# Kernel tuning notes

Measured on AMD Instinct MI355X. Metric: run time of the kernel, lower is better.

The kernel has to match this reference:

```python
import jax, jax.numpy as jnp
import numpy as np
from jax import lax

D = 256      # key/query dim
D_F = 256    # diff feature channels
C_TOK = 1    # leading context tokens in query_vit
EPS = 1e-6


def conv2d(x, w, b, pad):
    out = lax.conv_general_dilated(x, w, (1, 1), [(pad, pad), (pad, pad)],
                                   dimension_numbers=('NCHW', 'OIHW', 'NCHW'))
    return out + b[None, :, None, None]


def gn1(x, g, b):
    # GroupNorm with 1 group: normalize over (C,H,W) per sample
    mu = jnp.mean(x, axis=(1, 2, 3), keepdims=True)
    var = jnp.var(x, axis=(1, 2, 3), keepdims=True)
    xn = (x - mu) * lax.rsqrt(var + EPS)
    return xn * g[None, :, None, None] + b[None, :, None, None]


def resize_bilinear_ac(x, Ho, Wo):
    # F.interpolate(mode='bilinear', align_corners=True)
    B, C, H, W = x.shape
    ys = jnp.linspace(0.0, H - 1.0, Ho)
    xs = jnp.linspace(0.0, W - 1.0, Wo)
    y0 = jnp.floor(ys).astype(jnp.int32)
    y1 = jnp.minimum(y0 + 1, H - 1)
    wy = (ys - y0)[None, None, :, None]
    x0 = jnp.floor(xs).astype(jnp.int32)
    x1 = jnp.minimum(x0 + 1, W - 1)
    wx = (xs - x0)[None, None, None, :]
    r = x[:, :, y0, :] * (1.0 - wy) + x[:, :, y1, :] * wy
    return r[:, :, :, x0] * (1.0 - wx) + r[:, :, :, x1] * wx


def setup_inputs() -> dict:
    key = jax.random.key(0)
    ks = jax.random.split(key, 12)
    B, Hd, Wd, Ht, Wt = 8, 64, 64, 32, 32

    def kaiming(k, shape, fan_in):
        return jax.random.normal(k, shape, jnp.float32) * np.sqrt(2.0 / fan_in)

    return {
        'query_vit': jax.random.normal(ks[0], (B, C_TOK + Ht * Wt, D), jnp.float32),
        'feat_diff_cat': jax.random.normal(ks[1], (B, 5 * D_F, Hd, Wd), jnp.float32),
        'rb_w1': kaiming(ks[2], (D_F, 5 * D_F, 3, 3), 5 * D_F * 9), 'rb_b1': jnp.zeros((D_F,), jnp.float32),
        'rb_w2': kaiming(ks[3], (D_F, D_F, 3, 3), D_F * 9), 'rb_b2': jnp.zeros((D_F,), jnp.float32),
        'rb_ws': kaiming(ks[4], (D_F, 5 * D_F, 1, 1), 5 * D_F), 'rb_bs': jnp.zeros((D_F,), jnp.float32),
        'ln_g': jnp.ones((D_F,), jnp.float32), 'ln_b': jnp.zeros((D_F,), jnp.float32),
        'key_w': kaiming(ks[5], (D, D_F, 1, 1), D_F), 'key_b': jnp.zeros((D,), jnp.float32),
        'val_w': kaiming(ks[6], (D_F, D_F, 1, 1), D_F), 'val_b': jnp.zeros((D_F,), jnp.float32),
        'dh0_w': kaiming(ks[7], (D_F, D_F, 3, 3), D_F * 9), 'dh0_b': jnp.zeros((D_F,), jnp.float32),
        'dh1_w': kaiming(ks[8], (D_F, D_F, 3, 3), D_F * 9), 'dh1_b': jnp.zeros((D_F,), jnp.float32),
    }


def reference(query_vit, feat_diff_cat, rb_w1, rb_b1, rb_w2, rb_b2, rb_ws, rb_bs,
              ln_g, ln_b, key_w, key_b, val_w, val_b, dh0_w, dh0_b, dh1_w, dh1_b):
    B, _, h_diff, w_diff = feat_diff_cat.shape
    N = query_vit.shape[1] - C_TOK
    h_trm = w_trm = int(N ** 0.5)

    # ResBlock_ysh(D_f*5 -> D_f): conv3x3 + relu + conv3x3, 1x1-projected residual
    h = jax.nn.relu(conv2d(feat_diff_cat, rb_w1, rb_b1, 1))
    h = conv2d(h, rb_w2, rb_b2, 1)
    feat_diff = jax.nn.relu(h + conv2d(feat_diff_cat, rb_ws, rb_bs, 0))

    fln = gn1(feat_diff, ln_g, ln_b)
    key_diff = conv2d(fln, key_w, key_b, 0).reshape(B, D, -1)          # (B, D, HW)
    value_diff = conv2d(fln, val_w, val_b, 0).reshape(B, D_F, -1)      # (B, Df, HW)
    value_diff = jnp.transpose(value_diff, (0, 2, 1))                  # (B, HW, Df)

    # cross attention: (B, C+N, D) @ (B, D, HW) -> softmax -> @ (B, HW, Df)
    scores = jnp.einsum('bnd,bdm->bnm', query_vit, key_diff) * (D ** -0.5)
    attn = jax.nn.softmax(scores, axis=-1)
    out_cross = jnp.einsum('bnm,bmf->bnf', attn, value_diff)           # (B, C+N, Df)

    out_cross_c = out_cross[:, :C_TOK, :]
    out_p = jnp.transpose(out_cross[:, C_TOK:, :], (0, 2, 1)).reshape(B, D_F, h_trm, w_trm)
    out_p = jax.nn.relu(conv2d(out_p, dh0_w, dh0_b, 1))
    out_p = resize_bilinear_ac(out_p, h_diff, w_diff)
    out_p = out_p + feat_diff                                          # DropPath(0) = identity
    out_p = jax.nn.relu(conv2d(gn1(out_p, ln_g, ln_b), dh1_w, dh1_b, 1)) + out_p
    return out_cross_c, out_p
```

## Files before the change

kernel.cpp:

```cpp
#include <hip/hip_runtime.h>
#include <cstdint>
#include <cstddef>

typedef __attribute__((ext_vector_type(4))) float     f32x4;
typedef __attribute__((ext_vector_type(8))) __bf16    bf16x8;
typedef __attribute__((ext_vector_type(8))) short     short8;
typedef __attribute__((ext_vector_type(4))) unsigned short u16x4;
typedef unsigned short u16;

__device__ __forceinline__ float b2f(u16 u) {
  unsigned x = ((unsigned)u) << 16;
  float f;
  __builtin_memcpy(&f, &x, 4);
  return f;
}
__device__ __forceinline__ u16 f2b(float f) {
  unsigned u;
  __builtin_memcpy(&u, &f, 4);
  return (u16)((u + 0x7FFFu + ((u >> 16) & 1u)) >> 16);
}

struct GP {
  const u16*  A;
  const u16*  B;
  const float* bias;
  const void* aux;
  void*       C;
  float*      out0;
  float*      st;
  long long   aBS, bBS, cBS, auxBS, biasBS;
  int Ktot, Mrows, ldc;
  int cin, logW, wpad, poff;
  float scale;
};

#define GLDS16(g, l)                                                        \
  __builtin_amdgcn_global_load_lds(                                         \
      (const void __attribute__((address_space(1)))*)(g),                   \
      (void __attribute__((address_space(3)))*)(l), 16, 0, 0)

struct G256 {
  const u16* A;
  const u16* B;
  u16* P;
  long long aBS;
  int Ktot, cin, logW, wpad, poff;
};

__global__ __launch_bounds__(512, 2) void k_gemm256(G256 gp) {
  const int tid = threadIdx.x;
  const int l = tid & 63, w = tid >> 6;
  const int lr = l & 15, lc = l >> 4;
  const int id = blockIdx.x;
  const int xcd = id & 7, slot = id >> 3;
  const int sp = xcd >> 2;
  const int u = (xcd & 3) * 32 + slot;
  const int mt = u & 15;
  const int b = u >> 4;
  const int m0 = mt << 8;
  const int wm = w >> 2, wn = w & 3;

  __shared__ __align__(16) u16 sm[4][16384];
  u16* smb = &sm[0][0];

  f32x4 acc[8][4];
#pragma unroll
  for (int i = 0; i < 8; ++i)
#pragma unroll
    for (int j = 0; j < 4; ++j) acc[i][j] = (f32x4){0.f, 0.f, 0.f, 0.f};

  const u16* Ab = gp.A + (size_t)b * gp.aBS;
  const u16* aS[2];
  const u16* bS[2];
#pragma unroll
  for (int j = 0; j < 2; ++j) {
    const int r = j * 128 + w * 16 + (l >> 2);
    const int p = m0 + r;
    const int y = p >> gp.logW, x = p & ((1 << gp.logW) - 1);
    const int sw = ((l & 3) ^ ((r >> 1) & 3)) << 3;
    aS[j] = Ab + (size_t)((y + gp.poff) * gp.wpad + (x + gp.poff)) * gp.cin + sw;
    bS[j] = gp.B + (size_t)r * gp.Ktot + sw;
  }

  const int NH = gp.Ktot >> 6;
  const int kt0h = sp * NH;
  int off = kt0h << 5;
  int tap = off / gp.cin;
  int kcS = off - tap * gp.cin;
  int dxS = tap % 3;
  int tapS = (tap / 3) * gp.wpad + dxS;
  int hgS = kt0h;

  auto stage = [&](int h) {
    const int hb = h & 3;
    const int kB = hgS << 5;
    const int kA = tapS * gp.cin + kcS;
    kcS += 32;
    if (kcS == gp.cin) {
      kcS = 0; ++dxS; ++tapS;
      if (dxS == 3) { dxS = 0; tapS += gp.wpad - 3; }
    }
    ++hgS;
    u16* base = smb + hb * 16384 + (w * 16) * 32 + l * 8;
    GLDS16(aS[0] + kA, base);
    GLDS16(aS[1] + kA, base + 4096);
    GLDS16(bS[0] + kB, base + 8192);
    GLDS16(bS[1] + kB, base + 12288);
  };

  stage(0);
  stage(1);
  stage(2);
  asm volatile("s_waitcnt vmcnt(8)" ::: "memory");
  __builtin_amdgcn_s_barrier();

  bf16x8 av[8], bv[4];
  {
    const char* b0 = (const char*)smb;
#pragma unroll
    for (int mi = 0; mi < 8; ++mi) {
      const int row = wm * 128 + mi * 16 + lr;
      av[mi] = *(const bf16x8*)(b0 + row * 64 + ((lc ^ ((row >> 1) & 3)) << 4));
    }
#pragma unroll
    for (int ni = 0; ni < 4; ++ni) {
      const int row = wn * 64 + ni * 16 + lr;
      bv[ni] = *(const bf16x8*)(b0 + 16384 + row * 64 +
                                ((lc ^ ((row >> 1) & 3)) << 4));
    }
  }

  for (int h = 0; h < NH; ++h) {
    if (h + 3 < NH) stage(h + 3);
    const int rem = NH - 1 - h;
    if (rem > 0) {
      if (rem > 2)
        asm volatile("s_waitcnt vmcnt(8)" ::: "memory");
      else if (rem == 2)
        asm volatile("s_waitcnt vmcnt(4)" ::: "memory");
      else
        asm volatile("s_waitcnt vmcnt(0)" ::: "memory");
      asm volatile("s_waitcnt lgkmcnt(0)" ::: "memory");
      __builtin_amdgcn_s_barrier();
    }

    const bool pf = (h + 1 < NH);
    const char* nxt = (const char*)smb + ((h + 1) & 3) * 32768;

#pragma unroll
    for (int mi = 0; mi < 8; ++mi) {
      const int row = wm * 128 + mi * 16 + lr;
      const int sw = (lc ^ ((row >> 1) & 3)) << 4;
#pragma unroll
      for (int ni = 0; ni < 4; ++ni)
        acc[mi][ni] = __builtin_amdgcn_mfma_f32_16x16x32_bf16(
            av[mi], bv[ni], acc[mi][ni], 0, 0, 0);
      if (pf) av[mi] = *(const bf16x8*)(nxt + row * 64 + sw);
    }
    if (pf) {
#pragma unroll
      for (int ni = 0; ni < 4; ++ni) {
        const int row = wn * 64 + ni * 16 + lr;
        bv[ni] = *(const bf16x8*)(nxt + 16384 + row * 64 +
                                  ((lc ^ ((row >> 1) & 3)) << 4));
      }
    }
  }

  u16* P = gp.P + ((size_t)sp * 128 + b * 16 + mt) * 65536;
#pragma unroll
  for (int mi = 0; mi < 8; ++mi)
#pragma unroll
    for (int ni = 0; ni < 4; ++ni) {
      const int ncol = wn * 64 + ni * 16 + lr;
      const int mloc = wm * 128 + mi * 16 + lc * 4;
#pragma unroll
      for (int r = 0; r < 4; ++r)
        P[(size_t)(mloc + r) * 256 + ncol] = f2b(acc[mi][ni][r]);
    }
}

__global__ __launch_bounds__(256) void k_reduceH1(const u16* __restrict__ P,
                                                  const float* __restrict__ bias,
                                                  u16* __restrict__ o) {
  const int i4 = blockIdx.x * 256 + threadIdx.x;
  const int flat = i4 << 2;
  const int n0 = flat & 255;
  const int mloc = (flat >> 8) & 255;
  const int gm = flat >> 16;
  const u16x4 a = *(const u16x4*)(P + (size_t)gm * 65536 + mloc * 256 + n0);
  const u16x4 c = *(const u16x4*)(P + (size_t)(128 + gm) * 65536 + mloc * 256 + n0);
  const f32x4 bb = *(const f32x4*)(bias + n0);
  const int batch = gm >> 4;
  const int mg = (gm & 15) * 256 + mloc;
  const int y = mg >> 6, x = mg & 63;
  u16x4 r;
#pragma unroll
  for (int k = 0; k < 4; ++k)
    r[k] = f2b(fmaxf(b2f(a[k]) + b2f(c[k]) + bb[k], 0.f));
  *(u16x4*)(o + ((size_t)batch * 4356 + (size_t)(y + 1) * 66 + x + 1) * 256 + n0) = r;
}

template <int AMODE, int CW>
__global__ __launch_bounds__(512, 2) void k_gemm8(GP gp) {
  const int tid = threadIdx.x;
  const int l = tid & 63, w = tid >> 6;
  const int b = blockIdx.z;
  const int m0 = blockIdx.x * 128;
  const int wm = w >> 2, wn = w & 3;
  const int lr = l & 15, lc = l >> 4;

  __shared__ __align__(16) u16 sm[2][24576];

  f32x4 acc[4][4];
#pragma unroll
  for (int i = 0; i < 4; ++i)
#pragma unroll
    for (int j = 0; j < 4; ++j) acc[i][j] = (f32x4){0.f, 0.f, 0.f, 0.f};

  const u16* Ab = gp.A + (size_t)b * gp.aBS;
  const u16* Bb = gp.B + (size_t)b * gp.bBS;
  const int scoff = (((tid & 7) ^ ((tid >> 3) & 7)) << 3);

  const u16* aP[2];
  const u16* aP2[2];
#pragma unroll
  for (int i = 0; i < 2; ++i) {
    const int p = m0 + i * 64 + (tid >> 3);
    const int y = p >> 6, x = p & 63;
    aP[i] = Ab + (size_t)(y * 66 + x) * gp.cin + scoff;
    if (AMODE == 2) {
      const u16* Xb = (const u16*)gp.aux + (size_t)b * gp.auxBS;
      aP2[i] = Xb + (size_t)((y + 1) * 66 + (x + 1)) * 1280 + scoff;
    }
  }
  const u16* bP[4];
#pragma unroll
  for (int i = 0; i < 4; ++i)
    bP[i] = Bb + (size_t)(i * 64 + (tid >> 3)) * gp.Ktot + scoff;

  const int NT = gp.Ktot >> 6;
  const int seg1t = (AMODE == 2) ? 36 : 0x7fffffff;
  int kcS = 0, tapS = 0, dxS = 0, nstg = 0;

  auto stage = [&](int buf) {
    const int kt = nstg++;
    const int kB = kt << 6;
    u16* sA = &sm[buf][0] + (w << 9);
    u16* sB = &sm[buf][8192] + (w << 9);
    if (AMODE == 2 && kt >= seg1t) {
      const int kA = (kt - seg1t) << 6;
      GLDS16(aP2[0] + kA, sA);
      GLDS16(aP2[1] + kA, sA + 4096);
    } else {
      const int kA = tapS * gp.cin + kcS;
      kcS += 64;
      if (kcS == gp.cin) {
        kcS = 0; ++dxS; ++tapS;
        if (dxS == 3) { dxS = 0; tapS += 63; }
      }
      GLDS16(aP[0] + kA, sA);
      GLDS16(aP[1] + kA, sA + 4096);
    }
    GLDS16(bP[0] + kB, sB);
    GLDS16(bP[1] + kB, sB + 4096);
    GLDS16(bP[2] + kB, sB + 8192);
    GLDS16(bP[3] + kB, sB + 12288);
  };

  stage(0);
  asm volatile("s_waitcnt vmcnt(0)" ::: "memory");
  __builtin_amdgcn_s_barrier();

  for (int t = 0; t < NT; ++t) {
    const int buf = t & 1;
    const u16* sAc = &sm[buf][0];
    const u16* sBc = &sm[buf][8192];
    if (t + 1 < NT) stage(buf ^ 1);

    bf16x8 av0[4], av1[4], bv0[4], bv1[4];
#pragma unroll
    for (int mi = 0; mi < 4; ++mi) {
      const int row = wm * 64 + mi * 16 + lr;
      av0[mi] = *(const bf16x8*)(sAc + row * 64 + (((0 + lc) ^ (row & 7)) << 3));
      av1[mi] = *(const bf16x8*)(sAc + row * 64 + (((4 + lc) ^ (row & 7)) << 3));
    }
#pragma unroll
    for (int ni = 0; ni < 4; ++ni) {
      const int row = wn * 64 + ni * 16 + lr;
      bv0[ni] = *(const bf16x8*)(sBc + row * 64 + (((0 + lc) ^ (row & 7)) << 3));
      bv1[ni] = *(const bf16x8*)(sBc + row * 64 + (((4 + lc) ^ (row & 7)) << 3));
    }
#pragma unroll
    for (int mi = 0; mi < 4; ++mi)
#pragma unroll
      for (int ni = 0; ni < 4; ++ni)
        acc[mi][ni] = __builtin_amdgcn_mfma_f32_16x16x32_bf16(
            av0[mi], bv0[ni], acc[mi][ni], 0, 0, 0);
#pragma unroll
    for (int mi = 0; mi < 4; ++mi)
#pragma unroll
      for (int ni = 0; ni < 4; ++ni)
        acc[mi][ni] = __builtin_amdgcn_mfma_f32_16x16x32_bf16(
            av1[mi], bv1[ni], acc[mi][ni], 0, 0, 0);
    asm volatile("s_waitcnt vmcnt(0)" ::: "memory");
    __builtin_amdgcn_s_barrier();
  }

  float lsum = 0.f, lsq = 0.f;
#pragma unroll
  for (int mi = 0; mi < 4; ++mi) {
#pragma unroll
    for (int ni = 0; ni < 4; ++ni) {
      const int ncol = wn * 64 + ni * 16 + lr;
      const int mbase = m0 + wm * 64 + mi * 16 + lc * 4;
      const float bv_ = gp.bias[ncol];
      if constexpr (CW == 8) {
        float* F = (float*)gp.C + (size_t)b * gp.cBS;
        u16* FB = (u16*)gp.out0 + (size_t)b * gp.cBS;
#pragma unroll
        for (int r = 0; r < 4; ++r) {
          float v = fmaxf(acc[mi][ni][r] + bv_, 0.f);
          const size_t idx = (size_t)(mbase + r) * 256 + ncol;
          F[idx] = v;
          FB[idx] = f2b(v);
          lsum += v;
          lsq += v * v;
        }
      } else {
        float* Cf =
            (float*)gp.C + (size_t)b * gp.cBS + (size_t)ncol * 4096 + mbase;
        const float* mid = (const float*)gp.aux + (size_t)b * gp.auxBS;
        f32x4 o;
#pragma unroll
        for (int r = 0; r < 4; ++r) {
          float v = fmaxf(acc[mi][ni][r] + bv_, 0.f);
          o[r] = v + mid[(size_t)(mbase + r) * 256 + ncol];
        }
        *(f32x4*)Cf = o;
      }
    }
  }
  if constexpr (CW == 8) {
    __syncthreads();
#pragma unroll
    for (int o = 32; o; o >>= 1) {
      lsum += __shfl_down(lsum, o);
      lsq += __shfl_down(lsq, o);
    }
    float* red = (float*)&sm[0][0];
    if (l == 0) { red[w * 2] = lsum; red[w * 2 + 1] = lsq; }
    __syncthreads();
    if (tid == 0) {
      float s = 0.f, s2 = 0.f;
#pragma unroll
      for (int k = 0; k < 8; ++k) { s += red[k * 2]; s2 += red[k * 2 + 1]; }
      atomicAdd(&gp.st[b * 2], s);
      atomicAdd(&gp.st[b * 2 + 1], s2);
    }
  }
}

template <int AMODE, int CW, bool RELU>
__global__ __launch_bounds__(256, 2) void k_gemm(GP gp) {
  const int tid = threadIdx.x;
  const int l = tid & 63, w = tid >> 6;
  const int b = blockIdx.z;
  const int m0 = blockIdx.x * 128, n0 = blockIdx.y * 128;
  const int wm = w >> 1, wn = w & 1;

  __shared__ __align__(16) u16 smA[128 * 64];
  __shared__ __align__(16) u16 smB[128 * 64];

  f32x4 acc[4][4];
#pragma unroll
  for (int i = 0; i < 4; ++i)
#pragma unroll
    for (int j = 0; j < 4; ++j) acc[i][j] = (f32x4){0.f, 0.f, 0.f, 0.f};

  const u16* Ab = gp.A + (size_t)b * gp.aBS;
  const u16* Bb = gp.B + (size_t)b * gp.bBS;

  const int scoff = (((l & 7) ^ (l >> 3)) << 3);

  const u16* aRow[4];
  const u16* bRow[4];
  u16* ldsA[4];
  u16* ldsB[4];
#pragma unroll
  for (int i = 0; i < 4; ++i) {
    const int r = w * 32 + i * 8 + (l >> 3);
    bRow[i] = Bb + (size_t)(n0 + r) * gp.Ktot + scoff;
    const int p = m0 + r;
    if (AMODE == 0) {
      const int pc = p < gp.Mrows ? p : gp.Mrows - 1;
      aRow[i] = Ab + (size_t)pc * gp.Ktot + scoff;
    } else {
      const int y = p >> gp.logW, x = p & ((1 << gp.logW) - 1);
      const int icoord = (y + gp.poff) * gp.wpad + (x + gp.poff);
      aRow[i] = Ab + (size_t)icoord * gp.cin + scoff;
    }
    ldsA[i] = smA + (w * 32 + i * 8) * 64;
    ldsB[i] = smB + (w * 32 + i * 8) * 64;
  }

  const int ktiles = gp.Ktot >> 6;
  int tap_off = 0, dx = 0, kc = 0;

  for (int kt = 0; kt < ktiles; ++kt) {
    int koffA;
    if (AMODE == 0)
      koffA = kt << 6;
    else
      koffA = tap_off * gp.cin + kc;
    const int koffB = kt << 6;
#pragma unroll
    for (int i = 0; i < 4; ++i) GLDS16(aRow[i] + koffA, ldsA[i]);
#pragma unroll
    for (int i = 0; i < 4; ++i) GLDS16(bRow[i] + koffB, ldsB[i]);

    if (AMODE == 1) {
      kc += 64;
      if (kc == gp.cin) {
        kc = 0;
        ++dx;
        ++tap_off;
        if (dx == 3) { dx = 0; tap_off += gp.wpad - 3; }
      }
    }

    __syncthreads();
#pragma unroll
    for (int ks = 0; ks < 2; ++ks) {
      bf16x8 av[4], bv[4];
      const int cc = (ks << 2) + (l >> 4);
#pragma unroll
      for (int mi = 0; mi < 4; ++mi) {
        const int row = wm * 64 + mi * 16 + (l & 15);
        av[mi] = *(const bf16x8*)((const char*)smA + (row << 7) +
                                  ((cc ^ (row & 7)) << 4));
      }
#pragma unroll
      for (int ni = 0; ni < 4; ++ni) {
        const int row = wn * 64 + ni * 16 + (l & 15);
        bv[ni] = *(const bf16x8*)((const char*)smB + (row << 7) +
                                  ((cc ^ (row & 7)) << 4));
      }
#pragma unroll
      for (int mi = 0; mi < 4; ++mi)
#pragma unroll
        for (int ni = 0; ni < 4; ++ni)
          acc[mi][ni] = __builtin_amdgcn_mfma_f32_16x16x32_bf16(
              av[mi], bv[ni], acc[mi][ni], 0, 0, 0);
    }
    __syncthreads();
  }

#pragma unroll
  for (int mi = 0; mi < 4; ++mi) {
#pragma unroll
    for (int ni = 0; ni < 4; ++ni) {
      const int ncol = n0 + wn * 64 + ni * 16 + (l & 15);
      const int mbase = m0 + wm * 64 + mi * 16 + ((l >> 4) << 2);
      const float bv_ =
          gp.bias ? gp.bias[(size_t)b * gp.biasBS + ncol] : 0.f;

      if constexpr (CW == 7) {
        u16* base = (u16*)gp.C;
        if (ncol < 256) {
#pragma unroll
          for (int r = 0; r < 4; ++r)
            base[(size_t)b * 1048576 + (size_t)(mbase + r) * 256 + ncol] =
                f2b(acc[mi][ni][r] + bv_);
        } else {
          u16x4 pk;
#pragma unroll
          for (int r = 0; r < 4; ++r) pk[r] = f2b(acc[mi][ni][r] + bv_);
          *(u16x4*)(base + 8388608 + (size_t)b * 1048576 +
                    (size_t)(ncol - 256) * 4096 + mbase) = pk;
        }
      } else {
#pragma unroll
        for (int reg = 0; reg < 4; ++reg) {
          const int mrow = mbase + reg;
          if (mrow >= gp.Mrows) continue;
          float v = acc[mi][ni][reg] * gp.scale + bv_;
          if (RELU) v = v > 0.f ? v : 0.f;
          if constexpr (CW == 0) {
            ((u16*)gp.C)[(size_t)b * gp.cBS + (size_t)mrow * gp.ldc + ncol] =
                f2b(v);
          } else if constexpr (CW == 5) {
            ((float*)gp.C)[(size_t)b * gp.cBS + (size_t)mrow * 256 + ncol] = v;
          }
        }
      }
    }
  }
}

__global__ __launch_bounds__(256, 2) void k_attnv(const u16* __restrict__ S,
                                                  const u16* __restrict__ Vv,
                                                  float* __restrict__ PAV) {
  const int tid = threadIdx.x;
  const int l = tid & 63, w = tid >> 6;
  const int b = blockIdx.z >> 2, sp = blockIdx.z & 3;
  const int m0 = blockIdx.x * 128, n0 = blockIdx.y * 128;
  const int wm = w >> 1, wn = w & 1;

  __shared__ __align__(16) u16 smA[128 * 64];
  __shared__ __align__(16) u16 smB[128 * 64];

  f32x4 acc[4][4];
#pragma unroll
  for (int i = 0; i < 4; ++i)
#pragma unroll
    for (int j = 0; j < 4; ++j) acc[i][j] = (f32x4){0.f, 0.f, 0.f, 0.f};

  const u16* Ab = S + (size_t)b * 4198400 + sp * 1024;
  const u16* Bb = Vv + (size_t)b * 1048576 + sp * 1024;
  const int scoff = (((l & 7) ^ (l >> 3)) << 3);

  const u16* aRow[4];
  const u16* bRow[4];
  u16* ldsA[4];
  u16* ldsB[4];
#pragma unroll
  for (int i = 0; i < 4; ++i) {
    const int r = w * 32 + i * 8 + (l >> 3);
    bRow[i] = Bb + (size_t)(n0 + r) * 4096 + scoff;
    const int p = m0 + r;
    const int pc = p < 1025 ? p : 1024;
    aRow[i] = Ab + (size_t)pc * 4096 + scoff;
    ldsA[i] = smA + (w * 32 + i * 8) * 64;
    ldsB[i] = smB + (w * 32 + i * 8) * 64;
  }

  for (int kt = 0; kt < 16; ++kt) {
    const int koff = kt << 6;
#pragma unroll
    for (int i = 0; i < 4; ++i) GLDS16(aRow[i] + koff, ldsA[i]);
#pragma unroll
    for (int i = 0; i < 4; ++i) GLDS16(bRow[i] + koff, ldsB[i]);

    __syncthreads();
#pragma unroll
    for (int ks = 0; ks < 2; ++ks) {
      bf16x8 av[4], bv[4];
      const int cc = (ks << 2) + (l >> 4);
#pragma unroll
      for (int mi = 0; mi < 4; ++mi) {
        const int row = wm * 64 + mi * 16 + (l & 15);
        av[mi] = *(const bf16x8*)((const char*)smA + (row << 7) +
                                  ((cc ^ (row & 7)) << 4));
      }
#pragma unroll
      for (int ni = 0; ni < 4; ++ni) {
        const int row = wn * 64 + ni * 16 + (l & 15);
        bv[ni] = *(const bf16x8*)((const char*)smB + (row << 7) +
                                  ((cc ^ (row & 7)) << 4));
      }
#pragma unroll
      for (int mi = 0; mi < 4; ++mi)
#pragma unroll
        for (int ni = 0; ni < 4; ++ni)
          acc[mi][ni] = __builtin_amdgcn_mfma_f32_16x16x32_bf16(
              av[mi], bv[ni], acc[mi][ni], 0, 0, 0);
    }
    __syncthreads();
  }

  float* P = PAV + (size_t)blockIdx.z * 262400;
#pragma unroll
  for (int mi = 0; mi < 4; ++mi) {
#pragma unroll
    for (int ni = 0; ni < 4; ++ni) {
      const int ncol = n0 + wn * 64 + ni * 16 + (l & 15);
      const int mbase = m0 + wm * 64 + mi * 16 + ((l >> 4) << 2);
#pragma unroll
      for (int r = 0; r < 4; ++r) {
        const int mrow = mbase + r;
        if (mrow >= 1025) continue;
        P[(size_t)mrow * 256 + ncol] = acc[mi][ni][r];
      }
    }
  }
}

__global__ __launch_bounds__(256) void k_reduceAttn(const float* __restrict__ PAV,
                                                    float* __restrict__ out0,
                                                    u16* __restrict__ OCP) {
  const int b = blockIdx.y;
  const int i4 = blockIdx.x * 256 + threadIdx.x;
  if (i4 >= 65600) return;
  const int flat = i4 << 2;
  const int row = flat >> 8;
  const int col = flat & 255;
  const float* base = PAV + (size_t)(b * 4) * 262400 + (size_t)row * 256 + col;
  f32x4 s = *(const f32x4*)base;
  s += *(const f32x4*)(base + 262400);
  s += *(const f32x4*)(base + 524800);
  s += *(const f32x4*)(base + 787200);
  if (row == 0) {
    *(f32x4*)(out0 + (size_t)b * 256 + col) = s;
  } else {
    const int p = row - 1, y = p >> 5, x = p & 31;
    u16x4 r;
#pragma unroll
    for (int k = 0; k < 4; ++k) r[k] = f2b(s[k]);
    *(u16x4*)(OCP + ((size_t)b * 1156 + (size_t)(y + 1) * 34 + x + 1) * 256 +
              col) = r;
  }
}


__global__ __launch_bounds__(256) void k_prep_x(const float* __restrict__ x,
                                                u16* __restrict__ o) {
  __shared__ float t[32][65];
  const int b = blockIdx.z, c0 = blockIdx.y << 5, y = blockIdx.x;
  const float* src = x + ((size_t)b * 1280 + c0) * 4096 + (size_t)y * 64;
#pragma unroll
  for (int i = 0; i < 8; ++i) {
    const int idx = threadIdx.x + (i << 8);
    const int c = idx >> 6, xx = idx & 63;
    t[c][xx] = src[(size_t)c * 4096 + xx];
  }
  __syncthreads();
  u16* dst = o + ((size_t)b * 4356 + (size_t)(y + 1) * 66 + 1) * 1280 + c0;
  const int xx = threadIdx.x >> 2;
  const int cq = (threadIdx.x & 3) << 3;
  short8 pk;
#pragma unroll
  for (int j = 0; j < 8; ++j) pk[j] = (short)f2b(t[cq + j][xx]);
  *(short8*)(dst + (size_t)xx * 1280 + cq) = pk;
}

__device__ __forceinline__ void zb1(u16* p, int P, int C, int idx) {
  const int per_img = (4 * P - 4) * C;
  const int b = idx / per_img;
  const int r = idx % per_img;
  const int pix = r / C, c = r % C;
  int y, x;
  const int Pm = P - 1;
  if (pix < P) { y = 0; x = pix; }
  else if (pix < 2 * P) { y = Pm; x = pix - P; }
  else if (pix < 3 * P - 2) { y = pix - 2 * P + 1; x = 0; }
  else { y = pix - (3 * P - 2) + 1; x = Pm; }
  p[((size_t)b * P * P + (size_t)y * P + x) * C + c] = 0;
}

__global__ __launch_bounds__(256) void k_zero_borders(u16* XPAD, u16* H1,
                                                      u16* G2, u16* OCP) {
  const int nx = 8 * 260 * 1280;
  const int nh = 8 * 260 * 256;
  const int no = 8 * 132 * 256;
  const int total = nx + 2 * nh + no;
  for (int i = blockIdx.x * 256 + threadIdx.x; i < total;
       i += gridDim.x * 256) {
    if (i < nx) zb1(XPAD, 66, 1280, i);
    else if (i < nx + nh) zb1(H1, 66, 256, i - nx);
    else if (i < nx + 2 * nh) zb1(G2, 66, 256, i - nx - nh);
    else zb1(OCP, 34, 256, i - nx - 2 * nh);
  }
}

__global__ __launch_bounds__(256) void k_prep_all(
    const float* __restrict__ w1, const float* __restrict__ w2,
    const float* __restrict__ wsc, const float* __restrict__ wd0,
    const float* __restrict__ wd1, const float* __restrict__ b2,
    const float* __restrict__ bsc, const float* __restrict__ q,
    u16* __restrict__ W1R, u16* __restrict__ WCAT2, u16* __restrict__ WD0R,
    u16* __restrict__ WD1R, float* __restrict__ BB2, u16* __restrict__ QB) {
  const int N1 = 2949120, N2 = 917504, N3 = 589824, N4 = 589824,
            N5 = 2099200, N6 = 256;
  const int T = N1 + N2 + N3 + N4 + N5 + N6;
  for (int i = blockIdx.x * 256 + threadIdx.x; i < T; i += gridDim.x * 256) {
    if (i < N1) {
      const int ci = i % 1280, r = i / 1280, t = r % 9, co = r / 9;
      W1R[i] = f2b(w1[((size_t)co * 1280 + ci) * 9 + t]);
    } else if (i < N1 + N2) {
      const int k = i - N1;
      const int co = k / 3584, kk = k % 3584;
      float v;
      if (kk < 2304) {
        const int tap = kk / 256, ci = kk % 256;
        v = w2[((size_t)co * 256 + ci) * 9 + tap];
      } else {
        v = wsc[(size_t)co * 1280 + (kk - 2304)];
      }
      WCAT2[k] = f2b(v);
    } else if (i < N1 + N2 + N3) {
      const int k = i - N1 - N2;
      const int ci = k % 256, r = k / 256, t = r % 9, co = r / 9;
      WD0R[k] = f2b(wd0[((size_t)co * 256 + ci) * 9 + t]);
    } else if (i < N1 + N2 + N3 + N4) {
      const int k = i - N1 - N2 - N3;
      const int ci = k % 256, r = k / 256, t = r % 9, co = r / 9;
      WD1R[k] = f2b(wd1[((size_t)co * 256 + ci) * 9 + t]);
    } else if (i < N1 + N2 + N3 + N4 + N5) {
      const int k = i - N1 - N2 - N3 - N4;
      QB[k] = f2b(q[k] * 0.0625f);
    } else {
      const int k = i - N1 - N2 - N3 - N4 - N5;
      BB2[k] = b2[k] + bsc[k];
    }
  }
}

__global__ __launch_bounds__(256) void k_foldkv(
    const float* __restrict__ wk, const float* __restrict__ wv,
    const float* __restrict__ bk, const float* __restrict__ bv,
    const float* __restrict__ g, const float* __restrict__ lnb,
    const float* __restrict__ st, u16* __restrict__ WKVB,
    float* __restrict__ BKVB) {
  const int idx = blockIdx.x * 256 + threadIdx.x;
  const int b = idx >> 9, j = idx & 511;
  const float mu = st[b * 2] * (1.f / 1048576.f);
  const float var = st[b * 2 + 1] * (1.f / 1048576.f) - mu * mu;
  const float rs = rsqrtf(var + 1e-6f);
  const float* wrow = (j < 256) ? wk + (size_t)j * 256 : wv + (size_t)(j - 256) * 256;
  float acc = (j < 256) ? bk[j] : bv[j - 256];
  u16* orow = WKVB + ((size_t)b * 512 + j) * 256;
  for (int c = 0; c < 256; ++c) {
    const float wv_ = wrow[c];
    orow[c] = f2b(wv_ * g[c] * rs);
    acc += wv_ * (lnb[c] - mu * rs * g[c]);
  }
  BKVB[b * 512 + j] = acc;
}

template <bool PAD>
__global__ __launch_bounds__(256) void k_gn_norm(const float* __restrict__ x,
                                                 const float* __restrict__ st,
                                                 const float* __restrict__ g,
                                                 const float* __restrict__ bb,
                                                 u16* __restrict__ o) {
  const int b = blockIdx.y;
  const float mu = st[b * 2] * (1.f / 1048576.f);
  const float var = st[b * 2 + 1] * (1.f / 1048576.f) - mu * mu;
  const float rs = rsqrtf(var + 1e-6f);
  const int i4 = blockIdx.x * 256 + threadIdx.x;
  const f32x4 v = ((const f32x4*)(x + (size_t)b * 1048576))[i4];
  const int flat = i4 << 2;
  const int c = flat & 255;
  const int p = flat >> 8;
  const f32x4 gv = *(const f32x4*)(g + c);
  const f32x4 bv = *(const f32x4*)(bb + c);
  u16x4 r;
#pragma unroll
  for (int k = 0; k < 4; ++k) r[k] = f2b((v[k] - mu) * rs * gv[k] + bv[k]);
  size_t oidx;
  if (PAD) {
    const int y = p >> 6, xx = p & 63;
    oidx = ((size_t)b * 4356 + (size_t)(y + 1) * 66 + xx + 1) * 256 + c;
  } else {
    oidx = ((size_t)b * 4096 + p) * 256 + c;
  }
  *(u16x4*)(o + oidx) = r;
}

__global__ __launch_bounds__(256) void k_softmax(u16* __restrict__ s) {
  const size_t row = blockIdx.x;
  u16* p = s + row * 4096;
  const int t = threadIdx.x;
  const short8 r0 = ((const short8*)p)[t];
  const short8 r1 = ((const short8*)p)[t + 256];
  float v[16];
#pragma unroll
  for (int i = 0; i < 8; ++i) {
    v[i] = b2f((u16)r0[i]);
    v[8 + i] = b2f((u16)r1[i]);
  }
  float m = v[0];
#pragma unroll
  for (int i = 1; i < 16; ++i) m = fmaxf(m, v[i]);
#pragma unroll
  for (int o = 32; o; o >>= 1) m = fmaxf(m, __shfl_xor(m, o));
  __shared__ float lm[4], lsum[4];
  const int w = t >> 6;
  if ((t & 63) == 0) lm[w] = m;
  __syncthreads();
  m = fmaxf(fmaxf(lm[0], lm[1]), fmaxf(lm[2], lm[3]));
  float sum = 0.f;
#pragma unroll
  for (int i = 0; i < 16; ++i) {
    v[i] = __expf(v[i] - m);
    sum += v[i];
  }
#pragma unroll
  for (int o = 32; o; o >>= 1) sum += __shfl_xor(sum, o);
  if ((t & 63) == 0) lsum[w] = sum;
  __syncthreads();
  sum = lsum[0] + lsum[1] + lsum[2] + lsum[3];
  const float inv = 1.f / sum;
  short8 o0, o1;
#pragma unroll
  for (int i = 0; i < 8; ++i) {
    o0[i] = (short)f2b(v[i] * inv);
    o1[i] = (short)f2b(v[8 + i] * inv);
  }
  ((short8*)p)[t] = o0;
  ((short8*)p)[t + 256] = o1;
}

__global__ __launch_bounds__(256) void k_resize_add(const float* __restrict__ d0,
                                                    const float* __restrict__ F,
                                                    float* __restrict__ mid,
                                                    float* __restrict__ st) {
  const int b = blockIdx.y;
  const float* db = d0 + (size_t)b * 262144;
  const float* Fb = F + (size_t)b * 1048576;
  float* mb = mid + (size_t)b * 1048576;
  float ls = 0.f, lq = 0.f;
  for (int i4 = blockIdx.x * 256 + threadIdx.x; i4 < 262144;
       i4 += 64 * 256) {
    const int flat = i4 << 2;
    const int c = flat & 255;
    const int p = flat >> 8;
    const int y = p >> 6, x = p & 63;
    const float fy = y * (31.f / 63.f);
    const int y0 = (int)fy;
    const float wy = fy - y0;
    const int y1 = y0 + 1 > 31 ? 31 : y0 + 1;
    const float fx = x * (31.f / 63.f);
    const int x0 = (int)fx;
    const float wx = fx - x0;
    const int x1 = x0 + 1 > 31 ? 31 : x0 + 1;
    const f32x4 a = *(const f32x4*)(db + ((size_t)(y0 * 32 + x0) << 8) + c);
    const f32x4 bq = *(const f32x4*)(db + ((size_t)(y0 * 32 + x1) << 8) + c);
    const f32x4 cq = *(const f32x4*)(db + ((size_t)(y1 * 32 + x0) << 8) + c);
    const f32x4 dq = *(const f32x4*)(db + ((size_t)(y1 * 32 + x1) << 8) + c);
    f32x4 r = (a * (1.f - wx) + bq * wx) * (1.f - wy) +
              (cq * (1.f - wx) + dq * wx) * wy;
    r += *(const f32x4*)(Fb + flat);
    *(f32x4*)(mb + flat) = r;
    ls += r[0] + r[1] + r[2] + r[3];
    lq += r[0] * r[0] + r[1] * r[1] + r[2] * r[2] + r[3] * r[3];
  }
#pragma unroll
  for (int o = 32; o; o >>= 1) {
    ls += __shfl_down(ls, o);
    lq += __shfl_down(lq, o);
  }
  __shared__ float red[8];
  const int w = threadIdx.x >> 6;
  if ((threadIdx.x & 63) == 0) { red[w * 2] = ls; red[w * 2 + 1] = lq; }
  __syncthreads();
  if (threadIdx.x == 0) {
    atomicAdd(&st[16 + b * 2], red[0] + red[2] + red[4] + red[6]);
    atomicAdd(&st[16 + b * 2 + 1], red[1] + red[3] + red[5] + red[7]);
  }
}


extern "C" void kernel_launch(void* const* d_in, const int* in_sizes, int n_in,
                              void* d_out, int out_size, void* d_ws,
                              size_t ws_size, hipStream_t stream) {
  (void)in_sizes; (void)n_in; (void)out_size;

  const float* q   = (const float*)d_in[0];
  const float* xdc = (const float*)d_in[1];
  const float* w1  = (const float*)d_in[2];
  const float* b1  = (const float*)d_in[3];
  const float* w2  = (const float*)d_in[4];
  const float* b2  = (const float*)d_in[5];
  const float* wsc = (const float*)d_in[6];
  const float* bsc = (const float*)d_in[7];
  const float* lng = (const float*)d_in[8];
  const float* lnb = (const float*)d_in[9];
  const float* wk  = (const float*)d_in[10];
  const float* bk  = (const float*)d_in[11];
  const float* wv  = (const float*)d_in[12];
  const float* bv  = (const float*)d_in[13];
  const float* wd0 = (const float*)d_in[14];
  const float* bd0 = (const float*)d_in[15];
  const float* wd1 = (const float*)d_in[16];
  const float* bd1 = (const float*)d_in[17];

  char* ws = (char*)d_ws;
  size_t cur = 0;
  auto alloc = [&](size_t sz) {
    char* p = ws + cur;
    cur += sz;
    return p;
  };
  u16* XPAD  = (u16*)alloc(89194496);
  u16* W1R   = (u16*)alloc(5898240);
  u16* WCAT2 = (u16*)alloc(1835008);
  u16* WD0R  = (u16*)alloc(1179648);
  u16* WD1R  = (u16*)alloc(1179648);
  u16* WKVB  = (u16*)alloc(2097152);
  float* BKVB = (float*)alloc(16384);
  float* BB2 = (float*)alloc(1024);
  u16* H1    = (u16*)alloc(17842176);
  float* F   = (float*)alloc(33554432);
  u16* FB    = (u16*)alloc(16777216);
  u16* KT    = (u16*)alloc(16777216);
  u16* V     = (u16*)alloc(16777216);
  u16* QB    = (u16*)alloc(4198400);
  u16* OCP   = (u16*)alloc(4734976);
  float* D0O = (float*)alloc(8388608);
  float* MID = (float*)alloc(33554432);
  u16* G2    = (u16*)alloc(17842176);
  float* ST  = (float*)alloc(256);
  u16* SCORES = XPAD;
  u16* PART = (u16*)F;
  float* PAV  = D0O;
  (void)V;

  if (ws_size < cur) return;

  float* out0 = (float*)d_out;
  float* out1 = (float*)d_out + 2048;

  hipMemsetAsync(ST, 0, 256, stream);
  k_zero_borders<<<2048, 256, 0, stream>>>(XPAD, H1, G2, OCP);
  k_prep_x<<<dim3(64, 40, 8), 256, 0, stream>>>(xdc, XPAD);
  k_prep_all<<<4096, 256, 0, stream>>>(w1, w2, wsc, wd0, wd1, b2, bsc, q, W1R,
                                       WCAT2, WD0R, WD1R, BB2, QB);

  {
    G256 g{};
    g.A = XPAD; g.B = W1R; g.P = PART;
    g.aBS = 5575680; g.Ktot = 11520;
    g.cin = 1280; g.logW = 6; g.wpad = 66; g.poff = 0;
    k_gemm256<<<256, 512, 0, stream>>>(g);
    k_reduceH1<<<8192, 256, 0, stream>>>(PART, b1, H1);
  }
  {
    GP g{};
    g.A = H1; g.B = WCAT2; g.bias = BB2; g.aux = XPAD; g.C = F;
    g.out0 = (float*)FB; g.st = ST;
    g.aBS = 1115136; g.bBS = 0; g.cBS = 1048576; g.auxBS = 5575680;
    g.Ktot = 3584; g.Mrows = 4096; g.ldc = 256;
    g.cin = 256; g.logW = 6; g.wpad = 66; g.poff = 0; g.scale = 1.f;
    k_gemm8<2, 8><<<dim3(32, 1, 8), 512, 0, stream>>>(g);
  }
  k_foldkv<<<16, 256, 0, stream>>>(wk, wv, bk, bv, lng, lnb, ST, WKVB, BKVB);
  {
    GP g{};
    g.A = FB; g.B = WKVB; g.bias = BKVB; g.C = KT;
    g.aBS = 1048576; g.bBS = 131072; g.cBS = 0; g.biasBS = 512;
    g.Ktot = 256; g.Mrows = 4096; g.ldc = 256; g.scale = 1.f;
    k_gemm<0, 7, false><<<dim3(32, 4, 8), 256, 0, stream>>>(g);
  }
  {
    GP g{};
    g.A = QB; g.B = KT; g.bias = nullptr; g.C = SCORES;
    g.aBS = 262400; g.bBS = 1048576; g.cBS = 4198400;
    g.Ktot = 256; g.Mrows = 1025; g.ldc = 4096; g.scale = 1.f;
    k_gemm<0, 0, false><<<dim3(9, 32, 8), 256, 0, stream>>>(g);
  }
  k_softmax<<<8200, 256, 0, stream>>>(SCORES);
  k_attnv<<<dim3(9, 2, 32), 256, 0, stream>>>(SCORES, V, PAV);
  k_reduceAttn<<<dim3(257, 8), 256, 0, stream>>>(PAV, out0, OCP);
  {
    GP g{};
    g.A = OCP; g.B = WD0R; g.bias = bd0; g.C = D0O;
    g.aBS = 295936; g.bBS = 0; g.cBS = 262144; g.biasBS = 0;
    g.Ktot = 2304; g.Mrows = 1024; g.ldc = 256;
    g.cin = 256; g.logW = 5; g.wpad = 34; g.poff = 0; g.scale = 1.f;
    k_gemm<1, 5, true><<<dim3(8, 2, 8), 256, 0, stream>>>(g);
  }
  k_resize_add<<<dim3(64, 8), 256, 0, stream>>>(D0O, F, MID, ST);
  k_gn_norm<true><<<dim3(1024, 8), 256, 0, stream>>>(MID, ST + 16, lng, lnb, G2);
  {
    GP g{};
    g.A = G2; g.B = WD1R; g.bias = bd1; g.C = out1; g.aux = MID;
    g.aBS = 1115136; g.bBS = 0; g.cBS = 1048576; g.auxBS = 1048576;
    g.Ktot = 2304; g.Mrows = 4096; g.ldc = 256;
    g.cin = 256; g.logW = 6; g.wpad = 66; g.poff = 0; g.scale = 1.f;
    k_gemm8<1, 6><<<dim3(32, 1, 8), 512, 0, stream>>>(g);
  }
}
```

Measured before the change: 661.6 us.

## Load GEMM B operand directly into registers, bypassing LDS staging

The weight (B) tiles of the implicit-GEMM conv kernel are no longer staged through shared memory. Each wave now reads its B fragments straight from global memory into registers, double-buffered one k-step ahead. This halves LDS use and removes the LDS reads for B. The A-tile prefetch depth drops from three stages to two, and each iteration ends with a full vmcnt(0) wait plus a barrier. In exchange, waves that share the same B columns now issue redundant global loads, and the shallower pipeline with full waits may expose more memory latency.

```diff
diff --git a/kernel.cpp b/kernel.cpp
--- a/kernel.cpp
+++ b/kernel.cpp
@@ -60,7 +60,7 @@
   const int m0 = mt << 8;
   const int wm = w >> 2, wn = w & 3;
 
-  __shared__ __align__(16) u16 sm[4][16384];
+  __shared__ __align__(16) u16 sm[4][8192];
   u16* smb = &sm[0][0];
 
   f32x4 acc[8][4];
@@ -71,7 +71,6 @@
 
   const u16* Ab = gp.A + (size_t)b * gp.aBS;
   const u16* aS[2];
-  const u16* bS[2];
 #pragma unroll
   for (int j = 0; j < 2; ++j) {
     const int r = j * 128 + w * 16 + (l >> 2);
@@ -79,8 +78,11 @@
     const int y = p >> gp.logW, x = p & ((1 << gp.logW) - 1);
     const int sw = ((l & 3) ^ ((r >> 1) & 3)) << 3;
     aS[j] = Ab + (size_t)((y + gp.poff) * gp.wpad + (x + gp.poff)) * gp.cin + sw;
-    bS[j] = gp.B + (size_t)r * gp.Ktot + sw;
-  }
+  }
+  const u16* bRowP[4];
+#pragma unroll
+  for (int ni = 0; ni < 4; ++ni)
+    bRowP[ni] = gp.B + (size_t)(wn * 64 + ni * 16 + lr) * gp.Ktot + lc * 8;
 
   const int NH = gp.Ktot >> 6;
   const int kt0h = sp * NH;
@@ -89,32 +91,30 @@
   int kcS = off - tap * gp.cin;
   int dxS = tap % 3;
   int tapS = (tap / 3) * gp.wpad + dxS;
-  int hgS = kt0h;
 
   auto stage = [&](int h) {
     const int hb = h & 3;
-    const int kB = hgS << 5;
     const int kA = tapS * gp.cin + kcS;
     kcS += 32;
     if (kcS == gp.cin) {
       kcS = 0; ++dxS; ++tapS;
       if (dxS == 3) { dxS = 0; tapS += gp.wpad - 3; }
     }
-    ++hgS;
-    u16* base = smb + hb * 16384 + (w * 16) * 32 + l * 8;
+    u16* base = smb + hb * 8192 + (w * 16) * 32 + l * 8;
     GLDS16(aS[0] + kA, base);
     GLDS16(aS[1] + kA, base + 4096);
-    GLDS16(bS[0] + kB, base + 8192);
-    GLDS16(bS[1] + kB, base + 12288);
   };
 
   stage(0);
   stage(1);
-  stage(2);
-  asm volatile("s_waitcnt vmcnt(8)" ::: "memory");
+  bf16x8 bv[4], bvN[4];
+#pragma unroll
+  for (int ni = 0; ni < 4; ++ni)
+    bv[ni] = *(const bf16x8*)(bRowP[ni] + ((size_t)kt0h << 5));
+  asm volatile("s_waitcnt vmcnt(0)" ::: "memory");
   __builtin_amdgcn_s_barrier();
 
-  bf16x8 av[8], bv[4];
+  bf16x8 av[8];
   {
     const char* b0 = (const char*)smb;
 #pragma unroll
@@ -122,31 +122,21 @@
       const int row = wm * 128 + mi * 16 + lr;
       av[mi] = *(const bf16x8*)(b0 + row * 64 + ((lc ^ ((row >> 1) & 3)) << 4));
     }
-#pragma unroll
-    for (int ni = 0; ni < 4; ++ni) {
-      const int row = wn * 64 + ni * 16 + lr;
-      bv[ni] = *(const bf16x8*)(b0 + 16384 + row * 64 +
-                                ((lc ^ ((row >> 1) & 3)) << 4));
-    }
-  }
+  }
+  asm volatile("s_waitcnt lgkmcnt(0)" ::: "memory");
+  __builtin_amdgcn_s_barrier();
 
   for (int h = 0; h < NH; ++h) {
-    if (h + 3 < NH) stage(h + 3);
-    const int rem = NH - 1 - h;
-    if (rem > 0) {
-      if (rem > 2)
-        asm volatile("s_waitcnt vmcnt(8)" ::: "memory");
-      else if (rem == 2)
-        asm volatile("s_waitcnt vmcnt(4)" ::: "memory");
-      else
-        asm volatile("s_waitcnt vmcnt(0)" ::: "memory");
-      asm volatile("s_waitcnt lgkmcnt(0)" ::: "memory");
-      __builtin_amdgcn_s_barrier();
-    }
-
     const bool pf = (h + 1 < NH);
-    const char* nxt = (const char*)smb + ((h + 1) & 3) * 32768;
-
+    if (h + 2 < NH) stage(h + 2);
+    if (pf) {
+      const size_t kB = (size_t)(kt0h + h + 1) << 5;
+#pragma unroll
+      for (int ni = 0; ni < 4; ++ni)
+        bvN[ni] = *(const bf16x8*)(bRowP[ni] + kB);
+    }
+
+    const char* nxt = (const char*)smb + ((h + 1) & 3) * 16384;
 #pragma unroll
     for (int mi = 0; mi < 8; ++mi) {
       const int row = wm * 128 + mi * 16 + lr;
@@ -159,11 +149,10 @@
     }
     if (pf) {
 #pragma unroll
-      for (int ni = 0; ni < 4; ++ni) {
-        const int row = wn * 64 + ni * 16 + lr;
-        bv[ni] = *(const bf16x8*)(nxt + 16384 + row * 64 +
-                                  ((lc ^ ((row >> 1) & 3)) << 4));
-      }
+      for (int ni = 0; ni < 4; ++ni) bv[ni] = bvN[ni];
+      asm volatile("s_waitcnt vmcnt(0)" ::: "memory");
+      asm volatile("s_waitcnt lgkmcnt(0)" ::: "memory");
+      __builtin_amdgcn_s_barrier();
     }
   }
 
```

New measurement: 841.7 us. +27.2%, slower.
